# Optimization experiments

Hardware: AMD Instinct MI355X
Metric: run time of the kernel (lower is better)

Reference implementation:

```python
import jax, jax.numpy as jnp
import numpy as np

PATCH = 2      # patch_size
NQ = 4         # n_qubits (state vector has 2**NQ amplitudes)
NL = 2         # n_layers
IMG = 28
NB = IMG // PATCH          # 14 patch blocks per side
NP = NB * NB               # 196 patches


def _bc(c, ndim):
    # broadcast a (B,P) or scalar coefficient against the remaining wire axes
    return c.reshape(c.shape + (1,) * (ndim - c.ndim)) if jnp.ndim(c) else c


def _apply_ry(state, theta, w):
    # state: (B, P, 2,2,2,2); theta: scalar or (B, P)
    st = jnp.moveaxis(state, 2 + w, -1)
    s0, s1 = st[..., 0], st[..., 1]
    h = theta * 0.5
    c = _bc(jnp.cos(h), s0.ndim)
    s = _bc(jnp.sin(h), s0.ndim)
    st = jnp.stack([c * s0 - s * s1, s * s0 + c * s1], axis=-1)
    return jnp.moveaxis(st, -1, 2 + w)


def _apply_rz(state, theta, w):
    st = jnp.moveaxis(state, 2 + w, -1)
    ph = _bc(jnp.exp(-0.5j * theta), st[..., 0].ndim)  # e^{-i theta/2}
    st = jnp.stack([ph * st[..., 0], jnp.conj(ph) * st[..., 1]], axis=-1)
    return jnp.moveaxis(st, -1, 2 + w)


def _apply_cnot(state, cw, tw):
    # control wire cw, target wire tw (cw < tw)
    st = jnp.moveaxis(state, (2 + cw, 2 + tw), (-2, -1))
    c0 = st[..., 0, :]
    c1 = jnp.stack([st[..., 1, 1], st[..., 1, 0]], axis=-1)  # flip target when control=1
    st = jnp.stack([c0, c1], axis=-2)
    return jnp.moveaxis(st, (-2, -1), (2 + cw, 2 + tw))


def _simulate(angles, var_params):
    # angles: (B, NP, NQ) encoder RY angles (pixel values); var_params: (NL, 2, NQ)
    B, P, _ = angles.shape
    state = jnp.zeros((B, P, 2 ** NQ), jnp.complex64).at[:, :, 0].set(1.0)
    state = state.reshape((B, P) + (2,) * NQ)
    for w in range(NQ):                       # GeneralEncoder: RY(x_i) on wire i
        state = _apply_ry(state, angles[:, :, w], w)
    for l in range(NL):                       # variational layers
        for w in range(NQ):
            state = _apply_ry(state, var_params[l, 0, w], w)
        for w in range(NQ):
            state = _apply_rz(state, var_params[l, 1, w], w)
        for c in range(NQ - 1):               # CNOT entanglement chain
            state = _apply_cnot(state, c, c + 1)
    probs = state.real ** 2 + state.imag ** 2  # (B, P, 2,2,2,2)
    exps = []
    for w in range(NQ):                        # <Z_w> = P(bit_w=0) - P(bit_w=1)
        other = tuple(2 + k for k in range(NQ) if k != w)
        p = probs.sum(axis=other)              # (B, P, 2)
        exps.append(p[..., 0] - p[..., 1])
    return jnp.stack(exps, axis=-1)            # (B, P, NQ)


def setup_inputs() -> dict:
    key = jax.random.key(0)
    k1, k2, k3 = jax.random.split(key, 3)
    B = 2048
    x = jax.random.uniform(k1, (B, IMG, IMG), dtype=jnp.float32)
    var_params = jax.random.normal(k2, (NL, 2, NQ), dtype=jnp.float32)
    W = jax.random.normal(k3, (10, NP * NQ), dtype=jnp.float32) * 0.03
    b = jnp.zeros((10,), dtype=jnp.float32)
    return {"x": x, "var_params": var_params, "W": W, "b": b}


def reference(x, var_params, W, b):
    B = x.shape[0]
    # extract non-overlapping PATCHxPATCH patches, row-major within patch
    patches = x.reshape(B, NB, PATCH, NB, PATCH).transpose(0, 1, 3, 2, 4)
    patches = patches.reshape(B, NP, PATCH * PATCH)
    meas = _simulate(patches, var_params)      # (B, NP, NQ)
    feats = meas.reshape(B, NP * NQ)           # patch-major concat, matches torch.cat
    logits = feats @ W.T + b
    return jax.nn.log_softmax(logits, axis=-1)
```

## Files before the change

### kernel.cpp

```cpp
#include <hip/hip_runtime.h>
#include <math.h>

#define NCLS 10


template<int STRIDE>
__device__ __forceinline__ void ry_cplx2(float2* a, float c, float s) {
    #pragma unroll
    for (int g = 0; g < 8; ++g) {
        const int lo = g & (STRIDE - 1);
        const int s0 = ((g ^ lo) << 1) | lo;
        const int s1 = s0 | STRIDE;
        const float2 a0 = a[s0], a1 = a[s1];
        a[s0] = make_float2(c * a0.x - s * a1.x, c * a0.y - s * a1.y);
        a[s1] = make_float2(s * a0.x + c * a1.x, s * a0.y + c * a1.y);
    }
}

template<int SC, int ST>
__device__ __forceinline__ void cnot2(float2* a) {
    #pragma unroll
    for (int idx = 0; idx < 16; ++idx) {
        if ((idx & SC) && !(idx & ST)) {
            const int j = idx | ST;
            const float2 tmp = a[idx]; a[idx] = a[j]; a[j] = tmp;
        }
    }
}

__global__ __launch_bounds__(256)
void quanv_fused(const float* __restrict__ x, const float* __restrict__ vp,
                 const float* __restrict__ W, const float* __restrict__ bias,
                 float* __restrict__ out) {
    __shared__ float2 ph2[16];
    __shared__ float ry1c[4], ry1s[4];
    __shared__ float4 feats4[196];
    __shared__ float logitsS[NCLS];

    const int b = blockIdx.x;
    const int t = threadIdx.x;

    if (t >= 224 && t < 244) {
        const int u = t - 224;
        float vc, vs;
        if (u < 16) {
            const float* rz = vp + 4;
            float phi = ((u & 8) ? 0.5f : -0.5f) * rz[0]
                      + ((u & 4) ? 0.5f : -0.5f) * rz[1]
                      + ((u & 2) ? 0.5f : -0.5f) * rz[2]
                      + ((u & 1) ? 0.5f : -0.5f) * rz[3];
            __sincosf(phi, &vs, &vc);
            ph2[u] = make_float2(vc, vs);
        } else {
            const int w = u - 16;
            __sincosf(0.5f * vp[8 + w], &vs, &vc);
            ry1c[w] = vc; ry1s[w] = vs;
        }
    }

    const bool is_sim = (t < 196);
    float sr[16];
    if (is_sim) {
        const int i = t / 14;
        const int j = t - i * 14;
        const float* xb = x + b * 784 + 2 * i * 28 + 2 * j;
        const float2 A  = *(const float2*)xb;
        const float2 Bv = *(const float2*)(xb + 28);

        float ec[4], es[4];
        __sincosf(0.5f * (A.x  + vp[0]), &es[0], &ec[0]);
        __sincosf(0.5f * (A.y  + vp[1]), &es[1], &ec[1]);
        __sincosf(0.5f * (Bv.x + vp[2]), &es[2], &ec[2]);
        __sincosf(0.5f * (Bv.y + vp[3]), &es[3], &ec[3]);

        float p01[4], p23[4];
        p01[0] = ec[0] * ec[1]; p01[1] = ec[0] * es[1];
        p01[2] = es[0] * ec[1]; p01[3] = es[0] * es[1];
        p23[0] = ec[2] * ec[3]; p23[1] = ec[2] * es[3];
        p23[2] = es[2] * ec[3]; p23[3] = es[2] * es[3];
        #pragma unroll
        for (int s = 0; s < 16; ++s) sr[s] = p01[s >> 2] * p23[s & 3];
    }
    __syncthreads();

    if (is_sim) {
        float2 a[16];
        #pragma unroll
        for (int k = 0; k < 16; ++k) {
            const float2 ph = ph2[k];
            a[k] = make_float2(sr[k] * ph.x, sr[k] * ph.y);
        }
        cnot2<8, 4>(a);
        cnot2<4, 2>(a);
        cnot2<2, 1>(a);

        ry_cplx2<8>(a, ry1c[0], ry1s[0]);
        ry_cplx2<4>(a, ry1c[1], ry1s[1]);
        ry_cplx2<2>(a, ry1c[2], ry1s[2]);
        ry_cplx2<1>(a, ry1c[3], ry1s[3]);

        float p[16];
        #pragma unroll
        for (int k = 0; k < 16; ++k) p[k] = a[k].x * a[k].x + a[k].y * a[k].y;

        float s8[8], d8[8];
        #pragma unroll
        for (int k = 0; k < 8; ++k) { s8[k] = p[2*k] + p[2*k+1]; d8[k] = p[2*k] - p[2*k+1]; }
        const float e3 =  d8[0] - d8[1] - d8[2] + d8[3] - d8[4] + d8[5] + d8[6] - d8[7];
        const float e2 =  s8[0] - s8[1] - s8[2] + s8[3] - s8[4] + s8[5] + s8[6] - s8[7];
        const float S0 = s8[0] + s8[1], S1 = s8[2] + s8[3], S2 = s8[4] + s8[5], S3 = s8[6] + s8[7];
        const float e1 = S0 - S1 - S2 + S3;
        const float e0 = S0 + S1 - S2 - S3;

        feats4[t] = make_float4(e0, e1, e2, e3);
    }
    __syncthreads();

    const int c = t >> 4, j = t & 15;
    float acc = 0.0f;
    if (c < NCLS) {
        const float4* __restrict__ W4 = (const float4*)W;
        #pragma unroll
        for (int i2 = 0; i2 < 12; ++i2) {
            const int v = j + 16 * i2;
            const float4 f = feats4[v];
            const float4 w = W4[c * 196 + v];
            acc += f.x * w.x + f.y * w.y + f.z * w.z + f.w * w.w;
        }
        if (j < 4) {
            const int v = j + 192;
            const float4 f = feats4[v];
            const float4 w = W4[c * 196 + v];
            acc += f.x * w.x + f.y * w.y + f.z * w.z + f.w * w.w;
        }
    }
    acc += __shfl_down(acc, 8, 16);
    acc += __shfl_down(acc, 4, 16);
    acc += __shfl_down(acc, 2, 16);
    acc += __shfl_down(acc, 1, 16);
    if (j == 0 && c < NCLS) logitsS[c] = acc + bias[c];
    __syncthreads();

    if (t < NCLS) {
        float m = -1e30f;
        #pragma unroll
        for (int k = 0; k < NCLS; ++k) m = fmaxf(m, logitsS[k]);
        float ssum = 0.0f;
        #pragma unroll
        for (int k = 0; k < NCLS; ++k) ssum += __expf(logitsS[k] - m);
        out[b * NCLS + t] = logitsS[t] - m - __logf(ssum);
    }
}

extern "C" void kernel_launch(void* const* d_in, const int* in_sizes, int n_in,
                              void* d_out, int out_size, void* d_ws, size_t ws_size,
                              hipStream_t stream) {
    const float* x  = (const float*)d_in[0];
    const float* vp = (const float*)d_in[1];
    const float* W  = (const float*)d_in[2];
    const float* bb = (const float*)d_in[3];
    float* out = (float*)d_out;

    quanv_fused<<<2048, 256, 0, stream>>>(x, vp, W, bb, out);
}
```

Measured before the change: 70.84 us.

## Replace statevector simulation with closed-form trig polynomial for expectations

The per-patch 16-amplitude complex statevector simulation (phases, CNOT swaps, RY rotations, probability reductions) is replaced by a closed-form expression. Each Z expectation becomes a sum of products of cos/sin of the full encoder angles, weighted by 30 coefficients that one thread derives from the variational parameters. This removes most per-thread arithmetic and register pressure. In exchange, correctness depends entirely on a hand-derived expansion, and the coefficient setup is serialized on a single thread.

```diff
diff --git a/kernel.cpp b/kernel.cpp
--- a/kernel.cpp
+++ b/kernel.cpp
@@ -4,114 +4,101 @@
 #define NCLS 10
 
 
-template<int STRIDE>
-__device__ __forceinline__ void ry_cplx2(float2* a, float c, float s) {
-    #pragma unroll
-    for (int g = 0; g < 8; ++g) {
-        const int lo = g & (STRIDE - 1);
-        const int s0 = ((g ^ lo) << 1) | lo;
-        const int s1 = s0 | STRIDE;
-        const float2 a0 = a[s0], a1 = a[s1];
-        a[s0] = make_float2(c * a0.x - s * a1.x, c * a0.y - s * a1.y);
-        a[s1] = make_float2(s * a0.x + c * a1.x, s * a0.y + c * a1.y);
-    }
-}
-
-template<int SC, int ST>
-__device__ __forceinline__ void cnot2(float2* a) {
-    #pragma unroll
-    for (int idx = 0; idx < 16; ++idx) {
-        if ((idx & SC) && !(idx & ST)) {
-            const int j = idx | ST;
-            const float2 tmp = a[idx]; a[idx] = a[j]; a[j] = tmp;
-        }
-    }
-}
-
 __global__ __launch_bounds__(256)
 void quanv_fused(const float* __restrict__ x, const float* __restrict__ vp,
                  const float* __restrict__ W, const float* __restrict__ bias,
                  float* __restrict__ out) {
-    __shared__ float2 ph2[16];
-    __shared__ float ry1c[4], ry1s[4];
+    __shared__ float K[30];
     __shared__ float4 feats4[196];
     __shared__ float logitsS[NCLS];
 
     const int b = blockIdx.x;
     const int t = threadIdx.x;
 
-    if (t >= 224 && t < 244) {
-        const int u = t - 224;
-        float vc, vs;
-        if (u < 16) {
-            const float* rz = vp + 4;
-            float phi = ((u & 8) ? 0.5f : -0.5f) * rz[0]
-                      + ((u & 4) ? 0.5f : -0.5f) * rz[1]
-                      + ((u & 2) ? 0.5f : -0.5f) * rz[2]
-                      + ((u & 1) ? 0.5f : -0.5f) * rz[3];
-            __sincosf(phi, &vs, &vc);
-            ph2[u] = make_float2(vc, vs);
-        } else {
-            const int w = u - 16;
-            __sincosf(0.5f * vp[8 + w], &vs, &vc);
-            ry1c[w] = vc; ry1s[w] = vs;
+    if (t == 224) {
+        float c1[4], s1[4], fx[4], fy[4];
+        #pragma unroll
+        for (int w = 0; w < 4; ++w) {
+            __sincosf(vp[8 + w], &s1[w], &c1[w]);
+            __sincosf(vp[4 + w], &fy[w], &fx[w]);
         }
+        K[0] = c1[0];
+        K[1] = -s1[0] * fx[0] * fx[1];
+        K[2] =  c1[0] * c1[1];
+        K[3] = -c1[0] * s1[1] * fx[1] * fx[2];
+        K[4] =  s1[0] * c1[1] * fy[0] * fy[1];
+        K[5] =  s1[0] * s1[1] * fx[0] * fx[2];
+        K[6]  =  c1[0] * c1[1] * c1[2];
+        K[7]  = -c1[0] * c1[1] * s1[2] * fx[2] * fx[3];
+        K[8]  =  c1[0] * s1[1] * c1[2] * fy[1] * fy[2];
+        K[9]  =  c1[0] * s1[1] * s1[2] * fx[1] * fx[3];
+        K[10] = -s1[0] * c1[1] * c1[2] * fx[0] * fx[1];
+        K[11] = -s1[0] * c1[1] * s1[2] * fy[0] * fy[1] * fx[2] * fx[3];
+        K[12] = -s1[0] * s1[1] * c1[2] * fy[0] * fy[2];
+        K[13] = -s1[0] * s1[1] * s1[2] * fx[0] * fx[3];
+        K[14] =  c1[0] * c1[1] * c1[2] * c1[3];
+        K[15] = -c1[0] * c1[1] * c1[2] * s1[3] * fx[3];
+        K[16] =  c1[0] * c1[1] * s1[2] * c1[3] * fy[2] * fy[3];
+        K[17] =  c1[0] * c1[1] * s1[2] * s1[3] * fx[2];
+        K[18] = -c1[0] * s1[1] * c1[2] * c1[3] * fx[1] * fx[2];
+        K[19] = -c1[0] * s1[1] * c1[2] * s1[3] * fy[1] * fy[2] * fx[3];
+        K[20] = -c1[0] * s1[1] * s1[2] * c1[3] * fy[1] * fy[3];
+        K[21] = -c1[0] * s1[1] * s1[2] * s1[3] * fx[1];
+        K[22] =  s1[0] * c1[1] * c1[2] * c1[3] * fy[0] * fy[1];
+        K[23] =  s1[0] * c1[1] * c1[2] * s1[3] * fx[0] * fx[1] * fx[3];
+        K[24] = -s1[0] * c1[1] * s1[2] * c1[3] * fx[0] * fx[1] * fy[2] * fy[3];
+        K[25] =  s1[0] * c1[1] * s1[2] * s1[3] * fy[0] * fy[1] * fx[2];
+        K[26] =  s1[0] * s1[1] * c1[2] * c1[3] * fx[0] * fx[2];
+        K[27] =  s1[0] * s1[1] * c1[2] * s1[3] * fy[0] * fy[2] * fx[3];
+        K[28] =  s1[0] * s1[1] * s1[2] * c1[3] * fy[0] * fy[3];
+        K[29] =  s1[0] * s1[1] * s1[2] * s1[3] * fx[0];
     }
 
     const bool is_sim = (t < 196);
-    float sr[16];
+    float cA[4], sA[4];
     if (is_sim) {
         const int i = t / 14;
         const int j = t - i * 14;
         const float* xb = x + b * 784 + 2 * i * 28 + 2 * j;
         const float2 A  = *(const float2*)xb;
         const float2 Bv = *(const float2*)(xb + 28);
-
-        float ec[4], es[4];
-        __sincosf(0.5f * (A.x  + vp[0]), &es[0], &ec[0]);
-        __sincosf(0.5f * (A.y  + vp[1]), &es[1], &ec[1]);
-        __sincosf(0.5f * (Bv.x + vp[2]), &es[2], &ec[2]);
-        __sincosf(0.5f * (Bv.y + vp[3]), &es[3], &ec[3]);
-
-        float p01[4], p23[4];
-        p01[0] = ec[0] * ec[1]; p01[1] = ec[0] * es[1];
-        p01[2] = es[0] * ec[1]; p01[3] = es[0] * es[1];
-        p23[0] = ec[2] * ec[3]; p23[1] = ec[2] * es[3];
-        p23[2] = es[2] * ec[3]; p23[3] = es[2] * es[3];
-        #pragma unroll
-        for (int s = 0; s < 16; ++s) sr[s] = p01[s >> 2] * p23[s & 3];
+        __sincosf(A.x  + vp[0], &sA[0], &cA[0]);
+        __sincosf(A.y  + vp[1], &sA[1], &cA[1]);
+        __sincosf(Bv.x + vp[2], &sA[2], &cA[2]);
+        __sincosf(Bv.y + vp[3], &sA[3], &cA[3]);
     }
     __syncthreads();
 
     if (is_sim) {
-        float2 a[16];
-        #pragma unroll
-        for (int k = 0; k < 16; ++k) {
-            const float2 ph = ph2[k];
-            a[k] = make_float2(sr[k] * ph.x, sr[k] * ph.y);
-        }
-        cnot2<8, 4>(a);
-        cnot2<4, 2>(a);
-        cnot2<2, 1>(a);
-
-        ry_cplx2<8>(a, ry1c[0], ry1s[0]);
-        ry_cplx2<4>(a, ry1c[1], ry1s[1]);
-        ry_cplx2<2>(a, ry1c[2], ry1s[2]);
-        ry_cplx2<1>(a, ry1c[3], ry1s[3]);
-
-        float p[16];
-        #pragma unroll
-        for (int k = 0; k < 16; ++k) p[k] = a[k].x * a[k].x + a[k].y * a[k].y;
-
-        float s8[8], d8[8];
-        #pragma unroll
-        for (int k = 0; k < 8; ++k) { s8[k] = p[2*k] + p[2*k+1]; d8[k] = p[2*k] - p[2*k+1]; }
-        const float e3 =  d8[0] - d8[1] - d8[2] + d8[3] - d8[4] + d8[5] + d8[6] - d8[7];
-        const float e2 =  s8[0] - s8[1] - s8[2] + s8[3] - s8[4] + s8[5] + s8[6] - s8[7];
-        const float S0 = s8[0] + s8[1], S1 = s8[2] + s8[3], S2 = s8[4] + s8[5], S3 = s8[6] + s8[7];
-        const float e1 = S0 - S1 - S2 + S3;
-        const float e0 = S0 + S1 - S2 - S3;
-
+        const float s01 = sA[0] * sA[1];
+        const float s23 = sA[2] * sA[3];
+        const float e0 = K[0] * cA[0] + K[1] * s01;
+        const float e1 = K[2] * cA[1] + K[3] * (cA[0] * sA[1] * sA[2])
+                       + K[4] * s01   + K[5] * (sA[0] * sA[2]);
+        const float e2 = K[6]  * (cA[0] * cA[2])
+                       + K[7]  * (cA[1] * s23)
+                       + K[8]  * (sA[1] * sA[2])
+                       + K[9]  * (cA[0] * sA[1] * sA[3])
+                       + K[10] * (s01 * cA[2])
+                       + K[11] * (s01 * s23)
+                       + K[12] * (sA[0] * cA[1] * sA[2])
+                       + K[13] * (sA[0] * sA[3]);
+        const float e3 = K[14] * (cA[1] * cA[3])
+                       + K[15] * (cA[0] * cA[2] * sA[3])
+                       + K[16] * (cA[0] * s23)
+                       + K[17] * (cA[1] * sA[2])
+                       + K[18] * (cA[0] * sA[1] * sA[2] * cA[3])
+                       + K[19] * (sA[1] * s23)
+                       + K[20] * (sA[1] * cA[2] * sA[3])
+                       + K[21] * (cA[0] * sA[1])
+                       + K[22] * (s01 * cA[3])
+                       + K[23] * (s01 * cA[2] * sA[3])
+                       + K[24] * (s01 * s23)
+                       + K[25] * (s01 * sA[2])
+                       + K[26] * (sA[0] * sA[2] * cA[3])
+                       + K[27] * (sA[0] * cA[1] * sA[2] * sA[3])
+                       + K[28] * (sA[0] * cA[1] * cA[2] * sA[3])
+                       + K[29] * sA[0];
         feats4[t] = make_float4(e0, e1, e2, e3);
     }
     __syncthreads();
```

After: 67.19 us. 5.1% less time.
